# Kernel tuning notes

Measured on AMD Instinct MI355X. Metric: run time of the kernel, lower is better.

The kernel has to match this reference:

```python
import jax, jax.numpy as jnp
import numpy as np

PC_RANGE = np.array([-20.0, -20.0, -2.3, 20.0, 20.0, 0.9], np.float32)
GRID = np.array([0.1, 0.1, 0.1], np.float32)
K = 5                      # kernel_size
C_IN, C_OUT = 128, 128
BS, G = 8, 2000
SPATIAL = tuple(int(s) for s in ((PC_RANGE[3:] - PC_RANGE[:3]) / GRID).astype(np.int32))  # (400,400,32)


def setup_inputs() -> dict:
    key = jax.random.key(0)
    k1, k2, k3 = jax.random.split(key, 3)
    instance_feature = jax.random.normal(k1, (BS, G, C_IN), jnp.float32)
    anchor = jax.random.uniform(k2, (BS, G, 3), jnp.float32)          # normalized xyz in [0,1)
    w = jax.random.normal(k3, (K ** 3, C_IN, C_OUT), jnp.float32) * 0.02  # SubMConv3d weight, flattened offsets
    return {"instance_feature": instance_feature, "anchor": anchor, "w": w}


def _voxel_indices(anchor):
    # cartesian(): map normalized anchor xyz into the pc_range box, then voxelize.
    lo = jnp.asarray(PC_RANGE[:3])
    hi = jnp.asarray(PC_RANGE[3:])
    xyz = anchor[..., :3] * (hi - lo) + lo                 # [bs, g, 3]
    idx = ((xyz - lo) / jnp.asarray(GRID)).astype(jnp.int32)
    return idx


def reference(instance_feature, anchor, w):
    bs, g, c = instance_feature.shape
    n = bs * g
    idx = _voxel_indices(anchor).reshape(n, 3)             # [n, 3] int32 voxel coords
    bidx = jnp.repeat(jnp.arange(bs, dtype=jnp.int32), g)  # [n]
    Dx, Dy, Dz = SPATIAL

    # Rulebook substitute: dense voxel -> point-id lookup (-1 = inactive).
    grid = jnp.full((bs, Dx, Dy, Dz), -1, jnp.int32)
    grid = grid.at[bidx, idx[:, 0], idx[:, 1], idx[:, 2]].set(jnp.arange(n, dtype=jnp.int32))

    feats = instance_feature.reshape(n, c)
    r = (K - 1) // 2
    ax = jnp.arange(-r, r + 1, dtype=jnp.int32)
    offs = jnp.stack(jnp.meshgrid(ax, ax, ax, indexing="ij"), -1).reshape(-1, 3)  # [K^3, 3]
    dims = jnp.asarray([Dx, Dy, Dz], jnp.int32)

    # Submanifold conv: gather neighbor features per kernel offset, matmul, accumulate.
    def step(acc, inp):
        off, wk = inp                                       # off [3], wk [Cin, Cout]
        nb = idx + off[None, :]                             # [n, 3]
        inb = jnp.all((nb >= 0) & (nb < dims[None, :]), axis=-1)
        nbc = jnp.clip(nb, 0, dims[None, :] - 1)
        j = grid[bidx, nbc[:, 0], nbc[:, 1], nbc[:, 2]]     # [n] neighbor point id or -1
        valid = inb & (j >= 0)
        fj = jnp.where(valid[:, None], feats[jnp.clip(j, 0, n - 1)], 0.0)  # [n, Cin]
        return acc + fj @ wk, None

    out0 = jnp.zeros((n, C_OUT), feats.dtype)
    out, _ = jax.lax.scan(step, out0, (offs, w))
    return out.reshape(bs, g, C_OUT)                        # output_proj = Identity
```

## Files before the change

kernel.cpp:

```cpp
#include <hip/hip_runtime.h>
#include <stdint.h>

#define BSZ 8
#define GQ 2000
#define NPTS (BSZ * GQ)
#define CH 128
#define TBL_BITS 16
#define TBL_SIZE (1 << TBL_BITS)
#define TBL_MASK (TBL_SIZE - 1)
#define ZG 8
#define HCAP 8
#define TM 16
#define AS_LD 129
#define KB 32
#define POISON ((int)0xAAAAAAAA)

#define WS_VALS 262144

__device__ __forceinline__ uint32_t hash_of(uint32_t k) {
    return (k * 2654435761u) >> (32 - TBL_BITS);
}

__device__ __forceinline__ int3 voxel_idx(const float* __restrict__ anchor, int i,
                                          float sx, float sy, float sz,
                                          float lx, float ly, float lz, float g) {
    float ax = anchor[i * 3 + 0];
    float ay = anchor[i * 3 + 1];
    float az = anchor[i * 3 + 2];
    float x = __fadd_rn(__fmul_rn(ax, sx), lx);
    float y = __fadd_rn(__fmul_rn(ay, sy), ly);
    float z = __fadd_rn(__fmul_rn(az, sz), lz);
    int ix = (int)__fdiv_rn(__fsub_rn(x, lx), g);
    int iy = (int)__fdiv_rn(__fsub_rn(y, ly), g);
    int iz = (int)__fdiv_rn(__fsub_rn(z, lz), g);
    return make_int3(ix, iy, iz);
}

__global__ void build_hash_kernel(const float* __restrict__ anchor,
                                  int* __restrict__ keys,
                                  int4* __restrict__ valtab,
                                  float sx, float sy, float sz,
                                  float lx, float ly, float lz, float g,
                                  int Dx, int Dy, int Dz) {
    int i = blockIdx.x * blockDim.x + threadIdx.x;
    if (i >= NPTS) return;
    int3 v = voxel_idx(anchor, i, sx, sy, sz, lx, ly, lz, g);
    if (v.x < 0 || v.x >= Dx || v.y < 0 || v.y >= Dy || v.z < 0 || v.z >= Dz) return;
    int b = i / GQ;
    int zg = v.z >> 2;
    int zi = v.z & 3;
    int key = ((b * Dx + v.x) * Dy + v.y) * ZG + zg;
    uint32_t slot = hash_of((uint32_t)key);
    for (;;) {
        int prev = atomicCAS(&keys[slot], POISON, key);
        if (prev == POISON || prev == key) {
            atomicMax(((int*)&valtab[slot]) + zi, i);
            break;
        }
        slot = (slot + 1) & TBL_MASK;
    }
}

__global__ void __launch_bounds__(256)
fused_kernel(const float* __restrict__ feat,
             const float* __restrict__ anchor,
             const float* __restrict__ w,
             const int* __restrict__ keys,
             const int4* __restrict__ valtab,
             float* __restrict__ out,
             float sx, float sy, float sz,
             float lx, float ly, float lz, float g,
             int Dx, int Dy, int Dz) {
    __shared__ float As[TM * AS_LD];
    __shared__ float Bs[KB * CH];
    __shared__ int4  vox[TM];
    __shared__ int   selfj[TM];
    __shared__ int   s_hn[TM];
    __shared__ int   s_hits[TM * HCAP];

    int rowbase = blockIdx.x * TM;
    int t = threadIdx.x;

    if (t < TM) {
        int i = rowbase + t;
        int3 v = voxel_idx(anchor, i, sx, sy, sz, lx, ly, lz, g);
        vox[t] = make_int4(v.x, v.y, v.z, i / GQ);
        selfj[t] = -1;
        s_hn[t] = 0;
    }
    __syncthreads();

    for (int f = t; f < TM * 50; f += 256) {
        int p = f / 50;
        int s = f - p * 50;
        int col = s >> 1;
        int gsel = s & 1;
        int4 v = vox[p];
        int ox = col / 5 - 2;
        int oy = col % 5 - 2;
        int nx = v.x + ox, ny = v.y + oy;
        if (nx < 0 || nx >= Dx || ny < 0 || ny >= Dy) continue;
        int zlo = v.z - 2; if (zlo < 0) zlo = 0;
        int zhi = v.z + 2; if (zhi > Dz - 1) zhi = Dz - 1;
        if (zlo > zhi) continue;
        int g0 = zlo >> 2, g1 = zhi >> 2;
        if (gsel == 1 && g1 == g0) continue;
        int zg = gsel ? g1 : g0;
        int key = ((v.w * Dx + nx) * Dy + ny) * ZG + zg;
        uint32_t slot = hash_of((uint32_t)key);
        int4 vals;
        bool found = false;
        for (;;) {
            int kk = keys[slot];
            if (kk == key) { vals = valtab[slot]; found = true; break; }
            if (kk < 0) break;
            slot = (slot + 1) & TBL_MASK;
        }
        if (!found) continue;
        int zbase = zg * 4;
        const int* vv = (const int*)&vals;
        #pragma unroll
        for (int c = 0; c < 4; ++c) {
            int z4 = zbase + c;
            if (z4 < zlo || z4 > zhi) continue;
            int j = vv[c];
            if (j < 0 || j >= NPTS) continue;
            int oz = z4 - v.z;
            int koff = (ox + 2) * 25 + (oy + 2) * 5 + (oz + 2);
            if (koff == 62) {
                selfj[p] = j;
            } else {
                int pos = atomicAdd(&s_hn[p], 1);
                if (pos < HCAP) s_hits[p * HCAP + pos] = (koff << 14) | j;
            }
        }
    }
    __syncthreads();

    #pragma unroll
    for (int f = t; f < TM * 32; f += 256) {
        int r = f >> 5;
        int c4 = f & 31;
        int j = selfj[r];
        float4 val = make_float4(0.f, 0.f, 0.f, 0.f);
        if (j >= 0) val = *(const float4*)(feat + (size_t)j * CH + c4 * 4);
        float* dst = As + r * AS_LD + c4 * 4;
        dst[0] = val.x; dst[1] = val.y; dst[2] = val.z; dst[3] = val.w;
    }

    int tc = t & 31;
    int tr = t >> 5;
    int r0 = tr * 2;

    float acc[2][4];
    #pragma unroll
    for (int a = 0; a < 2; ++a)
        #pragma unroll
        for (int b = 0; b < 4; ++b) acc[a][b] = 0.f;

    const float* B = w + (size_t)62 * CH * CH;

    #pragma unroll
    for (int chunk = 0; chunk < CH / KB; ++chunk) {
        __syncthreads();
        #pragma unroll
        for (int f = t; f < KB * 32; f += 256) {
            int kk = f >> 5;
            int c4 = f & 31;
            *(float4*)(Bs + kk * CH + c4 * 4) =
                *(const float4*)(B + (size_t)(chunk * KB + kk) * CH + c4 * 4);
        }
        __syncthreads();

        #pragma unroll 4
        for (int kk = 0; kk < KB; ++kk) {
            float4 b4 = *(const float4*)(Bs + kk * CH + tc * 4);
            float a0 = As[(r0 + 0) * AS_LD + chunk * KB + kk];
            float a1 = As[(r0 + 1) * AS_LD + chunk * KB + kk];
            acc[0][0] = fmaf(a0, b4.x, acc[0][0]); acc[0][1] = fmaf(a0, b4.y, acc[0][1]);
            acc[0][2] = fmaf(a0, b4.z, acc[0][2]); acc[0][3] = fmaf(a0, b4.w, acc[0][3]);
            acc[1][0] = fmaf(a1, b4.x, acc[1][0]); acc[1][1] = fmaf(a1, b4.y, acc[1][1]);
            acc[1][2] = fmaf(a1, b4.z, acc[1][2]); acc[1][3] = fmaf(a1, b4.w, acc[1][3]);
        }
    }

    #pragma unroll
    for (int rr = 0; rr < 2; ++rr) {
        int r = r0 + rr;
        int nh = s_hn[r];
        if (nh > HCAP) nh = HCAP;
        for (int h = 0; h < nh; ++h) {
            int packed = s_hits[r * HCAP + h];
            int k = packed >> 14;
            int j = packed & 0x3FFF;
            const float* fj = feat + (size_t)j * CH;
            const float* wk = w + (size_t)k * CH * CH + tc * 4;
            #pragma unroll 8
            for (int c = 0; c < CH; ++c) {
                float a = fj[c];
                float4 b4 = *(const float4*)(wk + (size_t)c * CH);
                acc[rr][0] = fmaf(a, b4.x, acc[rr][0]);
                acc[rr][1] = fmaf(a, b4.y, acc[rr][1]);
                acc[rr][2] = fmaf(a, b4.z, acc[rr][2]);
                acc[rr][3] = fmaf(a, b4.w, acc[rr][3]);
            }
        }
        int i = rowbase + r;
        float4 v = make_float4(acc[rr][0], acc[rr][1], acc[rr][2], acc[rr][3]);
        *(float4*)(out + (size_t)i * CH + tc * 4) = v;
    }
}

extern "C" void kernel_launch(void* const* d_in, const int* in_sizes, int n_in,
                              void* d_out, int out_size, void* d_ws, size_t ws_size,
                              hipStream_t stream) {
    const float* feat   = (const float*)d_in[0];
    const float* anchor = (const float*)d_in[1];
    const float* w      = (const float*)d_in[2];
    float* out = (float*)d_out;

    char* ws = (char*)d_ws;
    int*  keys   = (int*)ws;
    int4* valtab = (int4*)(ws + WS_VALS);

    float lx = -20.0f, ly = -20.0f, lz = -2.3f;
    float hx =  20.0f, hy =  20.0f, hz =  0.9f;
    float sx = hx - lx, sy = hy - ly, sz = hz - lz;
    float g = 0.1f;
    int Dx = (int)(sx / g);
    int Dy = (int)(sy / g);
    int Dz = (int)(sz / g);

    build_hash_kernel<<<(NPTS + 255) / 256, 256, 0, stream>>>(
        anchor, keys, valtab, sx, sy, sz, lx, ly, lz, g, Dx, Dy, Dz);

    fused_kernel<<<NPTS / TM, 256, 0, stream>>>(
        feat, anchor, w, keys, valtab, out, sx, sy, sz, lx, ly, lz, g, Dx, Dy, Dz);
}
```

Before: 105.0 us.

## Pack hash keys and 16-bit ids in one int4, shrink blocks, prefetch weights

Result: slower. 147.6 us (+40.6%).

```diff
diff --git a/kernel.cpp b/kernel.cpp
--- a/kernel.cpp
+++ b/kernel.cpp
@@ -10,12 +10,13 @@
 #define TBL_MASK (TBL_SIZE - 1)
 #define ZG 8
 #define HCAP 8
-#define TM 16
+#define TM 8
+#define NTHR 128
 #define AS_LD 129
 #define KB 32
-#define POISON ((int)0xAAAAAAAA)
-
-#define WS_VALS 262144
+#define POISON   ((int)0xAAAAAAAA)
+#define EMPTY16  0xAAAA
+
 
 __device__ __forceinline__ uint32_t hash_of(uint32_t k) {
     return (k * 2654435761u) >> (32 - TBL_BITS);
@@ -37,8 +38,7 @@
 }
 
 __global__ void build_hash_kernel(const float* __restrict__ anchor,
-                                  int* __restrict__ keys,
-                                  int4* __restrict__ valtab,
+                                  int4* __restrict__ tab,
                                   float sx, float sy, float sz,
                                   float lx, float ly, float lz, float g,
                                   int Dx, int Dy, int Dz) {
@@ -52,21 +52,31 @@
     int key = ((b * Dx + v.x) * Dy + v.y) * ZG + zg;
     uint32_t slot = hash_of((uint32_t)key);
     for (;;) {
-        int prev = atomicCAS(&keys[slot], POISON, key);
+        int* base = (int*)&tab[slot];
+        int prev = atomicCAS(base, POISON, key);
         if (prev == POISON || prev == key) {
-            atomicMax(((int*)&valtab[slot]) + zi, i);
+            int* wp = base + 1 + (zi >> 1);
+            int sh = (zi & 1) * 16;
+            int old = atomicAdd(wp, 0);
+            for (;;) {
+                int cur = (old >> sh) & 0xFFFF;
+                int nj = (cur == EMPTY16) ? i : (cur > i ? cur : i);
+                int neu = (old & ~(0xFFFF << sh)) | (nj << sh);
+                int got = atomicCAS(wp, old, neu);
+                if (got == old) break;
+                old = got;
+            }
             break;
         }
         slot = (slot + 1) & TBL_MASK;
     }
 }
 
-__global__ void __launch_bounds__(256)
+__global__ void __launch_bounds__(NTHR)
 fused_kernel(const float* __restrict__ feat,
              const float* __restrict__ anchor,
              const float* __restrict__ w,
-             const int* __restrict__ keys,
-             const int4* __restrict__ valtab,
+             const int4* __restrict__ tab,
              float* __restrict__ out,
              float sx, float sy, float sz,
              float lx, float ly, float lz, float g,
@@ -81,6 +91,15 @@
     int rowbase = blockIdx.x * TM;
     int t = threadIdx.x;
 
+    const float* B = w + (size_t)62 * CH * CH;
+
+    float4 breg[8];
+    #pragma unroll
+    for (int q = 0; q < 8; ++q) {
+        int f = t + q * NTHR;
+        breg[q] = *(const float4*)(B + (size_t)(f >> 5) * CH + (f & 31) * 4);
+    }
+
     if (t < TM) {
         int i = rowbase + t;
         int3 v = voxel_idx(anchor, i, sx, sy, sz, lx, ly, lz, g);
@@ -90,55 +109,76 @@
     }
     __syncthreads();
 
-    for (int f = t; f < TM * 50; f += 256) {
-        int p = f / 50;
-        int s = f - p * 50;
-        int col = s >> 1;
-        int gsel = s & 1;
+    {
+        int p = t >> 4;
+        int l16 = t & 15;
         int4 v = vox[p];
-        int ox = col / 5 - 2;
-        int oy = col % 5 - 2;
-        int nx = v.x + ox, ny = v.y + oy;
-        if (nx < 0 || nx >= Dx || ny < 0 || ny >= Dy) continue;
         int zlo = v.z - 2; if (zlo < 0) zlo = 0;
         int zhi = v.z + 2; if (zhi > Dz - 1) zhi = Dz - 1;
-        if (zlo > zhi) continue;
         int g0 = zlo >> 2, g1 = zhi >> 2;
-        if (gsel == 1 && g1 == g0) continue;
-        int zg = gsel ? g1 : g0;
-        int key = ((v.w * Dx + nx) * Dy + ny) * ZG + zg;
-        uint32_t slot = hash_of((uint32_t)key);
-        int4 vals;
-        bool found = false;
-        for (;;) {
-            int kk = keys[slot];
-            if (kk == key) { vals = valtab[slot]; found = true; break; }
-            if (kk < 0) break;
-            slot = (slot + 1) & TBL_MASK;
-        }
-        if (!found) continue;
-        int zbase = zg * 4;
-        const int* vv = (const int*)&vals;
-        #pragma unroll
-        for (int c = 0; c < 4; ++c) {
-            int z4 = zbase + c;
-            if (z4 < zlo || z4 > zhi) continue;
-            int j = vv[c];
-            if (j < 0 || j >= NPTS) continue;
-            int oz = z4 - v.z;
-            int koff = (ox + 2) * 25 + (oy + 2) * 5 + (oz + 2);
-            if (koff == 62) {
-                selfj[p] = j;
-            } else {
-                int pos = atomicAdd(&s_hn[p], 1);
-                if (pos < HCAP) s_hits[p * HCAP + pos] = (koff << 14) | j;
+
+        int tkey[4]; int tox[4], toy[4], tzg[4];
+        #pragma unroll
+        for (int it = 0; it < 4; ++it) {
+            int s = l16 + it * 16;
+            tkey[it] = -1;
+            if (s < 50 && zlo <= zhi) {
+                int col = s >> 1;
+                int gsel = s & 1;
+                int ox = col / 5 - 2;
+                int oy = col % 5 - 2;
+                int nx = v.x + ox, ny = v.y + oy;
+                bool ok = nx >= 0 && nx < Dx && ny >= 0 && ny < Dy &&
+                          !(gsel == 1 && g1 == g0);
+                if (ok) {
+                    int zg = gsel ? g1 : g0;
+                    tkey[it] = ((v.w * Dx + nx) * Dy + ny) * ZG + zg;
+                    tox[it] = ox; toy[it] = oy; tzg[it] = zg;
+                }
+            }
+        }
+        uint32_t slot[4];
+        int4 kv[4];
+        #pragma unroll
+        for (int it = 0; it < 4; ++it) {
+            slot[it] = hash_of((uint32_t)tkey[it]) & TBL_MASK;
+            kv[it] = tab[tkey[it] >= 0 ? slot[it] : 0];
+        }
+        #pragma unroll
+        for (int it = 0; it < 4; ++it) {
+            int key = tkey[it];
+            if (key < 0) continue;
+            int4 e = kv[it];
+            uint32_t sl = slot[it];
+            while (e.x != key && e.x >= 0) {
+                sl = (sl + 1) & TBL_MASK;
+                e = tab[sl];
+            }
+            if (e.x != key) continue;
+            int zbase = tzg[it] * 4;
+            int lane[4] = { e.y & 0xFFFF, (e.y >> 16) & 0xFFFF,
+                            e.z & 0xFFFF, (e.z >> 16) & 0xFFFF };
+            #pragma unroll
+            for (int c = 0; c < 4; ++c) {
+                int z4 = zbase + c;
+                if (z4 < zlo || z4 > zhi) continue;
+                int j = lane[c];
+                if (j >= NPTS) continue;
+                int oz = z4 - v.z;
+                int koff = (tox[it] + 2) * 25 + (toy[it] + 2) * 5 + (oz + 2);
+                if (koff == 62) {
+                    selfj[p] = j;
+                } else {
+                    int pos = atomicAdd(&s_hn[p], 1);
+                    if (pos < HCAP) s_hits[p * HCAP + pos] = (koff << 14) | j;
+                }
             }
         }
     }
     __syncthreads();
 
     #pragma unroll
-    for (int f = t; f < TM * 32; f += 256) {
+    for (int f = t; f < TM * 32; f += NTHR) {
         int r = f >> 5;
         int c4 = f & 31;
         int j = selfj[r];
@@ -158,20 +198,22 @@
         #pragma unroll
         for (int b = 0; b < 4; ++b) acc[a][b] = 0.f;
 
-    const float* B = w + (size_t)62 * CH * CH;
-
     #pragma unroll
     for (int chunk = 0; chunk < CH / KB; ++chunk) {
+        #pragma unroll
+        for (int q = 0; q < 8; ++q) {
+            int f = t + q * NTHR;
+            *(float4*)(Bs + (f >> 5) * CH + (f & 31) * 4) = breg[q];
+        }
         __syncthreads();
-        #pragma unroll
-        for (int f = t; f < KB * 32; f += 256) {
-            int kk = f >> 5;
-            int c4 = f & 31;
-            *(float4*)(Bs + kk * CH + c4 * 4) =
-                *(const float4*)(B + (size_t)(chunk * KB + kk) * CH + c4 * 4);
-        }
-        __syncthreads();
-
+        if (chunk < CH / KB - 1) {
+            #pragma unroll
+            for (int q = 0; q < 8; ++q) {
+                int f = t + q * NTHR;
+                breg[q] = *(const float4*)(B + (size_t)((chunk + 1) * KB + (f >> 5)) * CH
+                                             + (f & 31) * 4);
+            }
+        }
         #pragma unroll 4
         for (int kk = 0; kk < KB; ++kk) {
             float4 b4 = *(const float4*)(Bs + kk * CH + tc * 4);
@@ -182,6 +224,7 @@
             acc[1][0] = fmaf(a1, b4.x, acc[1][0]); acc[1][1] = fmaf(a1, b4.y, acc[1][1]);
             acc[1][2] = fmaf(a1, b4.z, acc[1][2]); acc[1][3] = fmaf(a1, b4.w, acc[1][3]);
         }
+        __syncthreads();
     }
 
     #pragma unroll
@@ -219,9 +262,7 @@
     const float* w      = (const float*)d_in[2];
     float* out = (float*)d_out;
 
-    char* ws = (char*)d_ws;
-    int*  keys   = (int*)ws;
-    int4* valtab = (int4*)(ws + WS_VALS);
+    int4* tab = (int4*)d_ws;
 
     float lx = -20.0f, ly = -20.0f, lz = -2.3f;
     float hx =  20.0f, hy =  20.0f, hz =  0.9f;
@@ -232,8 +273,8 @@
     int Dz = (int)(sz / g);
 
     build_hash_kernel<<<(NPTS + 255) / 256, 256, 0, stream>>>(
-        anchor, keys, valtab, sx, sy, sz, lx, ly, lz, g, Dx, Dy, Dz);
-
-    fused_kernel<<<NPTS / TM, 256, 0, stream>>>(
-        feat, anchor, w, keys, valtab, out, sx, sy, sz, lx, ly, lz, g, Dx, Dy, Dz);
-}
+        anchor, tab, sx, sy, sz, lx, ly, lz, g, Dx, Dy, Dz);
+
+    fused_kernel<<<NPTS / TM, NTHR, 0, stream>>>(
+        feat, anchor, w, tab, out, sx, sy, sz, lx, ly, lz, g, Dx, Dy, Dz);
+}
```

## Replace hash table with dense 16-bit voxel grid for neighbor lookup

Applied to the files above, without the earlier changes.

Result: faster. 101.5 us (-3.3%).

```diff
diff --git a/kernel.cpp b/kernel.cpp
--- a/kernel.cpp
+++ b/kernel.cpp
@@ -5,21 +5,14 @@
 #define GQ 2000
 #define NPTS (BSZ * GQ)
 #define CH 128
-#define TBL_BITS 16
-#define TBL_SIZE (1 << TBL_BITS)
-#define TBL_MASK (TBL_SIZE - 1)
-#define ZG 8
 #define HCAP 8
 #define TM 16
+#define NTHR 256
 #define AS_LD 129
 #define KB 32
-#define POISON ((int)0xAAAAAAAA)
-
-#define WS_VALS 262144
-
-__device__ __forceinline__ uint32_t hash_of(uint32_t k) {
-    return (k * 2654435761u) >> (32 - TBL_BITS);
-}
+#define ZPAD 32
+#define EMPTY16 0xAAAAu
+
 
 __device__ __forceinline__ int3 voxel_idx(const float* __restrict__ anchor, int i,
                                           float sx, float sy, float sz,
@@ -36,9 +29,8 @@
     return make_int3(ix, iy, iz);
 }
 
-__global__ void build_hash_kernel(const float* __restrict__ anchor,
-                                  int* __restrict__ keys,
-                                  int4* __restrict__ valtab,
+__global__ void build_grid_kernel(const float* __restrict__ anchor,
+                                  unsigned int* __restrict__ grid32,
                                   float sx, float sy, float sz,
                                   float lx, float ly, float lz, float g,
                                   int Dx, int Dy, int Dz) {
@@ -47,26 +39,26 @@
     int3 v = voxel_idx(anchor, i, sx, sy, sz, lx, ly, lz, g);
     if (v.x < 0 || v.x >= Dx || v.y < 0 || v.y >= Dy || v.z < 0 || v.z >= Dz) return;
     int b = i / GQ;
-    int zg = v.z >> 2;
-    int zi = v.z & 3;
-    int key = ((b * Dx + v.x) * Dy + v.y) * ZG + zg;
-    uint32_t slot = hash_of((uint32_t)key);
+    size_t cell = ((size_t)(b * Dx + v.x) * Dy + v.y) * ZPAD + v.z;
+    unsigned int* wp = grid32 + (cell >> 1);
+    int sh = (int)(cell & 1) * 16;
+    unsigned int old = *wp;
     for (;;) {
-        int prev = atomicCAS(&keys[slot], POISON, key);
-        if (prev == POISON || prev == key) {
-            atomicMax(((int*)&valtab[slot]) + zi, i);
-            break;
-        }
-        slot = (slot + 1) & TBL_MASK;
-    }
-}
-
-__global__ void __launch_bounds__(256)
+        unsigned int cur = (old >> sh) & 0xFFFFu;
+        unsigned int nj = (cur == EMPTY16) ? (unsigned int)i
+                          : (cur > (unsigned int)i ? cur : (unsigned int)i);
+        unsigned int neu = (old & ~(0xFFFFu << sh)) | (nj << sh);
+        unsigned int got = atomicCAS(wp, old, neu);
+        if (got == old) break;
+        old = got;
+    }
+}
+
+__global__ void __launch_bounds__(NTHR)
 fused_kernel(const float* __restrict__ feat,
              const float* __restrict__ anchor,
              const float* __restrict__ w,
-             const int* __restrict__ keys,
-             const int4* __restrict__ valtab,
+             const unsigned short* __restrict__ grid16,
              float* __restrict__ out,
              float sx, float sy, float sz,
              float lx, float ly, float lz, float g,
@@ -90,41 +82,32 @@
     }
     __syncthreads();
 
-    for (int f = t; f < TM * 50; f += 256) {
-        int p = f / 50;
-        int s = f - p * 50;
-        int col = s >> 1;
-        int gsel = s & 1;
+    for (int f = t; f < TM * 25; f += NTHR) {
+        int p = f / 25;
+        int col = f - p * 25;
         int4 v = vox[p];
         int ox = col / 5 - 2;
-        int oy = col % 5 - 2;
+        int oy = col - (col / 5) * 5 - 2;
         int nx = v.x + ox, ny = v.y + oy;
         if (nx < 0 || nx >= Dx || ny < 0 || ny >= Dy) continue;
         int zlo = v.z - 2; if (zlo < 0) zlo = 0;
         int zhi = v.z + 2; if (zhi > Dz - 1) zhi = Dz - 1;
         if (zlo > zhi) continue;
-        int g0 = zlo >> 2, g1 = zhi >> 2;
-        if (gsel == 1 && g1 == g0) continue;
-        int zg = gsel ? g1 : g0;
-        int key = ((v.w * Dx + nx) * Dy + ny) * ZG + zg;
-        uint32_t slot = hash_of((uint32_t)key);
-        int4 vals;
-        bool found = false;
-        for (;;) {
-            int kk = keys[slot];
-            if (kk == key) { vals = valtab[slot]; found = true; break; }
-            if (kk < 0) break;
-            slot = (slot + 1) & TBL_MASK;
-        }
-        if (!found) continue;
-        int zbase = zg * 4;
-        const int* vv = (const int*)&vals;
+        int g0 = zlo >> 2;
+        int g1 = g0 + 1; if (g1 > (ZPAD / 4 - 1)) g1 = ZPAD / 4 - 1;
+        size_t colbase = ((size_t)(v.w * Dx + nx) * Dy + ny) * ZPAD;
+        ushort4 q0 = *(const ushort4*)(grid16 + colbase + g0 * 4);
+        ushort4 q1 = *(const ushort4*)(grid16 + colbase + g1 * 4);
+        unsigned short e0 = q0.x, e1 = q0.y, e2 = q0.z, e3 = q0.w;
+        unsigned short e4 = q1.x, e5 = q1.y, e6 = q1.z, e7 = q1.w;
+        unsigned short ee[8] = {e0, e1, e2, e3, e4, e5, e6, e7};
+        int zbase = g0 * 4;
         #pragma unroll
-        for (int c = 0; c < 4; ++c) {
+        for (int c = 0; c < 8; ++c) {
             int z4 = zbase + c;
             if (z4 < zlo || z4 > zhi) continue;
-            int j = vv[c];
-            if (j < 0 || j >= NPTS) continue;
+            int j = ee[c];
+            if (j >= NPTS) continue;
             int oz = z4 - v.z;
             int koff = (ox + 2) * 25 + (oy + 2) * 5 + (oz + 2);
             if (koff == 62) {
@@ -138,7 +121,7 @@
     __syncthreads();
 
     #pragma unroll
-    for (int f = t; f < TM * 32; f += 256) {
+    for (int f = t; f < TM * 32; f += NTHR) {
         int r = f >> 5;
         int c4 = f & 31;
         int j = selfj[r];
@@ -164,7 +147,7 @@
     for (int chunk = 0; chunk < CH / KB; ++chunk) {
         __syncthreads();
         #pragma unroll
-        for (int f = t; f < KB * 32; f += 256) {
+        for (int f = t; f < KB * 32; f += NTHR) {
             int kk = f >> 5;
             int c4 = f & 31;
             *(float4*)(Bs + kk * CH + c4 * 4) =
@@ -219,9 +202,8 @@
     const float* w      = (const float*)d_in[2];
     float* out = (float*)d_out;
 
-    char* ws = (char*)d_ws;
-    int*  keys   = (int*)ws;
-    int4* valtab = (int4*)(ws + WS_VALS);
+    unsigned int*   grid32 = (unsigned int*)d_ws;
+    unsigned short* grid16 = (unsigned short*)d_ws;
 
     float lx = -20.0f, ly = -20.0f, lz = -2.3f;
     float hx =  20.0f, hy =  20.0f, hz =  0.9f;
@@ -231,9 +213,9 @@
     int Dy = (int)(sy / g);
     int Dz = (int)(sz / g);
 
-    build_hash_kernel<<<(NPTS + 255) / 256, 256, 0, stream>>>(
-        anchor, keys, valtab, sx, sy, sz, lx, ly, lz, g, Dx, Dy, Dz);
-
-    fused_kernel<<<NPTS / TM, 256, 0, stream>>>(
-        feat, anchor, w, keys, valtab, out, sx, sy, sz, lx, ly, lz, g, Dx, Dy, Dz);
-}
+    build_grid_kernel<<<(NPTS + 255) / 256, 256, 0, stream>>>(
+        anchor, grid32, sx, sy, sz, lx, ly, lz, g, Dx, Dy, Dz);
+
+    fused_kernel<<<NPTS / TM, NTHR, 0, stream>>>(
+        feat, anchor, w, grid16, out, sx, sy, sz, lx, ly, lz, g, Dx, Dy, Dz);
+}
```
